# Kernel optimization log

Measured on AMD Instinct MI355X. Metric: run time of the kernel, lower is better.

The kernel has to match this reference:

```python
import jax, jax.numpy as jnp
import numpy as np

N = 50000
E = 800000
IN_C = 512
HID = 256
NUM_CLASS = (10, 25, 16, 350)


def _glorot(key, shape):
    fan_in, fan_out = shape[0], shape[1]
    lim = float(np.sqrt(6.0 / (fan_in + fan_out)))
    return jax.random.uniform(key, shape, jnp.float32, -lim, lim)


def setup_inputs() -> dict:
    key = jax.random.key(0)
    ks = jax.random.split(key, 16)
    x = jax.random.normal(ks[0], (N, IN_C), jnp.float32)
    edge_index = jax.random.randint(ks[1], (2, E), 0, N, jnp.int32)
    inp = {"x": x, "edge_index": edge_index}
    # gc1
    inp["W1"] = _glorot(ks[2], (IN_C, HID)); inp["b1"] = jnp.zeros((HID,), jnp.float32)
    # four GCNConv heads
    names = ["type", "school", "time", "author"]
    for i, (nm, nc) in enumerate(zip(names, NUM_CLASS)):
        inp[f"Wg_{nm}"] = _glorot(ks[3 + i], (HID, nc))
        inp[f"bg_{nm}"] = jnp.zeros((nc,), jnp.float32)
        inp[f"Wc_{nm}"] = _glorot(ks[7 + i], (nc, nc))
        inp[f"bc_{nm}"] = jnp.zeros((nc,), jnp.float32)
    return inp


def gcn_conv(x, W, b, src, dst, n):
    # GCNConv: out = D^{-1/2} (A + I) D^{-1/2} (x W) + b, symmetric norm.
    xw = x @ W  # [N, out]
    ones = jnp.ones((src.shape[0],), xw.dtype)
    deg = jax.ops.segment_sum(ones, dst, num_segments=n) + 1.0  # +1 from self-loop
    dinv = jax.lax.rsqrt(deg)
    norm = dinv[src] * dinv[dst]  # [E]
    agg = jax.ops.segment_sum(xw[src] * norm[:, None], dst, num_segments=n)
    # self-loop contribution: norm_ii = dinv_i^2
    return agg + xw * (dinv * dinv)[:, None] + b


def reference(x, edge_index, W1, b1,
              Wg_type, bg_type, Wc_type, bc_type,
              Wg_school, bg_school, Wc_school, bc_school,
              Wg_time, bg_time, Wc_time, bc_time,
              Wg_author, bg_author, Wc_author, bc_author):
    src, dst = edge_index[0], edge_index[1]
    n = x.shape[0]
    h = jax.nn.relu(gcn_conv(x, W1, b1, src, dst, n))  # dropout is identity in eval

    def head(Wg, bg, Wc, bc):
        g = gcn_conv(h, Wg, bg, src, dst, n)
        return jax.nn.softmax(g @ Wc + bc, axis=-1)

    out_type = head(Wg_type, bg_type, Wc_type, bc_type)
    out_school = head(Wg_school, bg_school, Wc_school, bc_school)
    out_time = head(Wg_time, bg_time, Wc_time, bc_time)
    out_author = head(Wg_author, bg_author, Wc_author, bc_author)
    return (out_type, out_school, out_time, out_author)
```

## Files before the change

### kernel.cpp

```cpp
#include <hip/hip_runtime.h>
#include <hip/hip_bf16.h>
#include <cstdint>
#include <cstddef>
#include <math.h>

#define NN 50000
#define NE 800000
#define INC 512
#define HIDC 256
#define NBLK ((NN + 255) / 256)
#define NB_DEG ((NE + 255) / 256)
#define NB_TR2 ((350 * 350 + 255) / 256)

typedef __attribute__((ext_vector_type(8))) short s8v;
typedef __attribute__((ext_vector_type(4))) float f4v;

__device__ __forceinline__ float b2f(unsigned short u) {
    return __uint_as_float(((unsigned)u) << 16);
}
__device__ __forceinline__ unsigned short f2b(float f) {
    __hip_bfloat16 h = __float2bfloat16(f);
    return *reinterpret_cast<unsigned short*>(&h);
}

__global__ void k_front1(const int* __restrict__ dst, int* __restrict__ cnt,
                         const float* __restrict__ Wg3, const float* __restrict__ Wc3,
                         float* __restrict__ Wg3t, float* __restrict__ Wc3t)
{
    if (blockIdx.x < NB_DEG) {
        int i = blockIdx.x * 256 + threadIdx.x;
        if (i < NE) atomicAdd(&cnt[dst[i]], 1);
    } else {
        int t = (blockIdx.x - NB_DEG) * 256 + threadIdx.x;
        if (t < 256 * 350) { int k = t / 350, i = t - k * 350; Wg3t[i * 256 + k] = Wg3[t]; }
        if (t < 350 * 350) { int i = t / 350, j = t - i * 350; Wc3t[j * 350 + i] = Wc3[t]; }
    }
}

__global__ void k_front2(const int* __restrict__ cnt, int* __restrict__ excl,
                         int* __restrict__ bsum, float* __restrict__ dinv,
                         const float* __restrict__ W1,
                         const float* __restrict__ Wg0, const float* __restrict__ Wc0,
                         const float* __restrict__ bg0, const float* __restrict__ bc0,
                         const float* __restrict__ Wg1, const float* __restrict__ Wc1,
                         const float* __restrict__ bg1, const float* __restrict__ bc1,
                         const float* __restrict__ Wg2, const float* __restrict__ Wc2,
                         const float* __restrict__ bg2, const float* __restrict__ bc2,
                         const float* __restrict__ Wg3, const float* __restrict__ Wc3,
                         const float* __restrict__ bg3, const float* __restrict__ bc3,
                         const float* __restrict__ Wg3t, const float* __restrict__ Wc3t,
                         unsigned short* __restrict__ W1t, unsigned short* __restrict__ Wft,
                         float* __restrict__ bfv)
{
    __shared__ float shm[352];
    int tid = threadIdx.x;
    if (blockIdx.x < NBLK) {
        int* s = (int*)shm;
        int i = blockIdx.x * 256 + tid;
        int v = (i < NN) ? cnt[i] : 0;
        if (i < NN) dinv[i] = rsqrtf((float)v + 1.0f);
        s[tid] = v;
        __syncthreads();
        for (int off = 1; off < 256; off <<= 1) {
            int t = (tid >= off) ? s[tid - off] : 0;
            __syncthreads();
            s[tid] += t;
            __syncthreads();
        }
        if (i < NN) excl[i] = s[tid] - v;
        if (tid == 255) bsum[blockIdx.x] = s[255];
        return;
    }
    int b = blockIdx.x - NBLK;
    if (b < 512) {
        int t = b * 256 + tid;
        int c = t >> 9, k = t & 511;
        W1t[(size_t)c * 512 + k] = f2b(W1[(size_t)k * 256 + c]);
    } else if (b < 960) {
        int j = b - 512, k = tid;
        float s = 0.f;
        if (j < 350) {
            for (int i = tid; i < 350; i += 256) shm[i] = Wc3t[(size_t)j * 350 + i];
            __syncthreads();
            for (int i = 0; i < 350; ++i) s += Wg3t[i * 256 + k] * shm[i];
        } else if (j >= 352 && j < 362) {
            int jj = j - 352; for (int i = 0; i < 10; ++i) s += Wg0[k * 10 + i] * Wc0[i * 10 + jj];
        } else if (j >= 362 && j < 387) {
            int jj = j - 362; for (int i = 0; i < 25; ++i) s += Wg1[k * 25 + i] * Wc1[i * 25 + jj];
        } else if (j >= 387 && j < 403) {
            int jj = j - 387; for (int i = 0; i < 16; ++i) s += Wg2[k * 16 + i] * Wc2[i * 16 + jj];
        }
        Wft[(size_t)j * 256 + k] = f2b(s);
    } else {
        int j = (b - 960) * 256 + tid;
        if (j >= 448) return;
        float s = 0.f;
        if (j < 350)                  { s = bc3[j]; for (int i = 0; i < 350; ++i) s += bg3[i] * Wc3[(size_t)i * 350 + j]; }
        else if (j >= 352 && j < 362) { int jj = j - 352; s = bc0[jj]; for (int i = 0; i < 10; ++i) s += bg0[i] * Wc0[i * 10 + jj]; }
        else if (j >= 362 && j < 387) { int jj = j - 362; s = bc1[jj]; for (int i = 0; i < 25; ++i) s += bg1[i] * Wc1[i * 25 + jj]; }
        else if (j >= 387 && j < 403) { int jj = j - 387; s = bc2[jj]; for (int i = 0; i < 16; ++i) s += bg2[i] * Wc2[i * 16 + jj]; }
        bfv[j] = s;
    }
}

#define GEMM1_NB ((NN + 127) / 128)
__global__ __launch_bounds__(512) void k_front3(
    const float* __restrict__ X, const unsigned short* __restrict__ Bt,
    unsigned short* __restrict__ C,
    int* __restrict__ rowptr, const int* __restrict__ bsum, int M)
{
    __shared__ s8v As[1024];
    __shared__ s8v Bs[2048];
    const int t = threadIdx.x;

    if (blockIdx.x >= GEMM1_NB) {
        int* sred = (int*)As;
        int b = blockIdx.x - GEMM1_NB;
        int v = (t < b) ? bsum[t] : 0;
        for (int o = 32; o; o >>= 1) v += __shfl_xor(v, o);
        if ((t & 63) == 0) sred[t >> 6] = v;
        __syncthreads();
        int off = 0;
#pragma unroll
        for (int w = 0; w < 8; ++w) off += sred[w];
        if (t < 256) {
            int i = b * 256 + t;
            if (i < NN) rowptr[i] += off;
            if (i == 0) rowptr[NN] = NE;
        }
        return;
    }

    const int lane = t & 63, wv = t >> 6;
    const int row0 = blockIdx.x * 128;
    const int l15 = lane & 15, lq = lane >> 4, l7 = lane & 7;

    f4v acc[16] = {};
    for (int k0 = 0; k0 < 512; k0 += 64) {
#pragma unroll
        for (int s = 0; s < 2; ++s) {
            int c = s * 512 + t;
            int row = c >> 3, ch = c & 7;
            int chg = ch ^ (row & 7);
            int gr = row0 + row; if (gr >= M) gr = M - 1;
            const float* src = X + (size_t)gr * 512 + k0 + chg * 8;
            float4 a = *(const float4*)src;
            float4 b = *(const float4*)(src + 4);
            s8v o;
            o[0] = (short)f2b(a.x); o[1] = (short)f2b(a.y);
            o[2] = (short)f2b(a.z); o[3] = (short)f2b(a.w);
            o[4] = (short)f2b(b.x); o[5] = (short)f2b(b.y);
            o[6] = (short)f2b(b.z); o[7] = (short)f2b(b.w);
            As[c] = o;
        }
#pragma unroll
        for (int s = 0; s < 4; ++s) {
            int c = s * 512 + t;
            int colr = c >> 3, ch = c & 7;
            int chg = ch ^ (colr & 7);
            Bs[c] = *(const s8v*)(Bt + (size_t)colr * 512 + k0 + chg * 8);
        }
        __syncthreads();
#pragma unroll
        for (int kk = 0; kk < 2; ++kk) {
            s8v af = As[(wv * 16 + l15) * 8 + ((kk * 4 + lq) ^ l7)];
#pragma unroll
            for (int cf = 0; cf < 16; ++cf) {
                s8v bfr = Bs[(cf * 16 + l15) * 8 + ((kk * 4 + lq) ^ l7)];
                acc[cf] = __builtin_amdgcn_mfma_f32_16x16x32_bf16(af, bfr, acc[cf], 0, 0, 0);
            }
        }
        __syncthreads();
    }
#pragma unroll
    for (int cf = 0; cf < 16; ++cf)
#pragma unroll
        for (int r = 0; r < 4; ++r) {
            int row = row0 + wv * 16 + lq * 4 + r;
            if (row < M) C[(size_t)row * 256 + cf * 16 + l15] = f2b(acc[cf][r]);
        }
}

__global__ void k_fill(const int* __restrict__ src, const int* __restrict__ dst,
                       const int* __restrict__ rowptr, int* __restrict__ cursor,
                       int* __restrict__ col, int e) {
    int i = blockIdx.x * 256 + threadIdx.x;
    if (i >= e) return;
    int d = dst[i];
    int pos = rowptr[d] + atomicAdd(&cursor[d], 1);
    col[pos] = src[i];
}

template <bool RELU, bool BIAS>
__global__ __launch_bounds__(256) void k_gather2(
    const unsigned short* __restrict__ feat, const int* __restrict__ rowptr,
    const int* __restrict__ col, const float* __restrict__ dinv,
    const float* __restrict__ bias, unsigned short* __restrict__ out, int n)
{
    int unit = (blockIdx.x * 256 + threadIdx.x) >> 5;
    int l32 = threadIdx.x & 31;
    if (unit >= n) return;
    float di = dinv[unit];
    int p0 = rowptr[unit], p1 = rowptr[unit + 1];
    int deg = p1 - p0;
    int myc = 0; float mydj = 0.f;
    if (l32 < deg) { myc = col[p0 + l32]; mydj = dinv[myc]; }
    float acc[8] = {};
    int dmin = deg < 32 ? deg : 32;
    int base = threadIdx.x & 32;
#pragma unroll 8
    for (int q = 0; q < dmin; ++q) {
        int j = __shfl(myc, base + q);
        float dj = __shfl(mydj, base + q);
        s8v v = *(const s8v*)(feat + (size_t)j * HIDC + l32 * 8);
#pragma unroll
        for (int c = 0; c < 8; ++c) acc[c] += dj * b2f((unsigned short)v[c]);
    }
    for (int p = p0 + 32; p < p1; ++p) {
        int j = col[p];
        float dj = dinv[j];
        s8v v = *(const s8v*)(feat + (size_t)j * HIDC + l32 * 8);
#pragma unroll
        for (int c = 0; c < 8; ++c) acc[c] += dj * b2f((unsigned short)v[c]);
    }
    s8v sv = *(const s8v*)(feat + (size_t)unit * HIDC + l32 * 8);
    float dd = di * di;
    s8v o;
#pragma unroll
    for (int c = 0; c < 8; ++c) {
        float r = di * acc[c] + dd * b2f((unsigned short)sv[c]);
        if (BIAS) r += bias[l32 * 8 + c];
        if (RELU) r = fmaxf(r, 0.f);
        o[c] = (short)f2b(r);
    }
    *(s8v*)(out + (size_t)unit * HIDC + l32 * 8) = o;
}

__global__ __launch_bounds__(512) void gemm2_heads(
    const unsigned short* __restrict__ A, const unsigned short* __restrict__ Bt,
    const float* __restrict__ bfv,
    float* __restrict__ o0, float* __restrict__ o1,
    float* __restrict__ o2, float* __restrict__ o3, int M)
{
    __shared__ s8v As[1024];
    __shared__ s8v Bs[3584];
    const int t = threadIdx.x;
    const int lane = t & 63, wv = t >> 6;
    const int row0 = blockIdx.x * 128;
    const int l15 = lane & 15, lq = lane >> 4, l7 = lane & 7;

    f4v acc[28] = {};
    for (int k0 = 0; k0 < 256; k0 += 64) {
#pragma unroll
        for (int s = 0; s < 2; ++s) {
            int c = s * 512 + t;
            int row = c >> 3, ch = c & 7;
            int chg = ch ^ (row & 7);
            int gr = row0 + row; if (gr >= M) gr = M - 1;
            As[c] = *(const s8v*)(A + (size_t)gr * 256 + k0 + chg * 8);
        }
#pragma unroll
        for (int s = 0; s < 7; ++s) {
            int c = s * 512 + t;
            int colr = c >> 3, ch = c & 7;
            int chg = ch ^ (colr & 7);
            Bs[c] = *(const s8v*)(Bt + (size_t)colr * 256 + k0 + chg * 8);
        }
        __syncthreads();
#pragma unroll
        for (int kk = 0; kk < 2; ++kk) {
            s8v af = As[(wv * 16 + l15) * 8 + ((kk * 4 + lq) ^ l7)];
#pragma unroll
            for (int cf = 0; cf < 28; ++cf) {
                s8v bfr = Bs[(cf * 16 + l15) * 8 + ((kk * 4 + lq) ^ l7)];
                acc[cf] = __builtin_amdgcn_mfma_f32_16x16x32_bf16(af, bfr, acc[cf], 0, 0, 0);
            }
        }
        __syncthreads();
    }
#pragma unroll
    for (int cf = 0; cf < 28; ++cf) {
        float b = bfv[cf * 16 + l15];
#pragma unroll
        for (int r = 0; r < 4; ++r) acc[cf][r] += b;
    }
#pragma unroll
    for (int r = 0; r < 4; ++r) {
        int row = row0 + wv * 16 + lq * 4 + r;
        float m0 = -1e30f, m1 = -1e30f, m2 = -1e30f, m3 = -1e30f;
#pragma unroll
        for (int cf = 0; cf < 28; ++cf) {
            int colc = cf * 16 + l15;
            float xv = acc[cf][r];
            if (colc < 350) m0 = fmaxf(m0, xv);
            else if (colc >= 352 && colc < 362) m1 = fmaxf(m1, xv);
            else if (colc >= 362 && colc < 387) m2 = fmaxf(m2, xv);
            else if (colc >= 387 && colc < 403) m3 = fmaxf(m3, xv);
        }
#pragma unroll
        for (int o = 8; o; o >>= 1) {
            m0 = fmaxf(m0, __shfl_xor(m0, o));
            m1 = fmaxf(m1, __shfl_xor(m1, o));
            m2 = fmaxf(m2, __shfl_xor(m2, o));
            m3 = fmaxf(m3, __shfl_xor(m3, o));
        }
        float s0 = 0.f, s1 = 0.f, s2 = 0.f, s3 = 0.f;
#pragma unroll
        for (int cf = 0; cf < 28; ++cf) {
            int colc = cf * 16 + l15;
            float xv = acc[cf][r];
            float e = 0.f;
            if (colc < 350)                     { e = __expf(xv - m0); s0 += e; }
            else if (colc >= 352 && colc < 362) { e = __expf(xv - m1); s1 += e; }
            else if (colc >= 362 && colc < 387) { e = __expf(xv - m2); s2 += e; }
            else if (colc >= 387 && colc < 403) { e = __expf(xv - m3); s3 += e; }
            acc[cf][r] = e;
        }
#pragma unroll
        for (int o = 8; o; o >>= 1) {
            s0 += __shfl_xor(s0, o); s1 += __shfl_xor(s1, o);
            s2 += __shfl_xor(s2, o); s3 += __shfl_xor(s3, o);
        }
        float i0 = 1.f / s0, i1 = 1.f / s1, i2 = 1.f / s2, i3 = 1.f / s3;
        if (row < M) {
#pragma unroll
            for (int cf = 0; cf < 28; ++cf) {
                int colc = cf * 16 + l15;
                float e = acc[cf][r];
                if (colc < 350)                     o3[(size_t)row * 350 + colc]       = e * i0;
                else if (colc >= 352 && colc < 362) o0[(size_t)row * 10 + colc - 352]  = e * i1;
                else if (colc >= 362 && colc < 387) o1[(size_t)row * 25 + colc - 362]  = e * i2;
                else if (colc >= 387 && colc < 403) o2[(size_t)row * 16 + colc - 387]  = e * i3;
            }
        }
    }
}

extern "C" void kernel_launch(void* const* d_in, const int* in_sizes, int n_in,
                              void* d_out, int out_size, void* d_ws, size_t ws_size,
                              hipStream_t stream)
{
    const float* x   = (const float*)d_in[0];
    const int*   ei  = (const int*)d_in[1];
    const float* W1  = (const float*)d_in[2];
    const float* b1  = (const float*)d_in[3];
    const float* Wg0 = (const float*)d_in[4];
    const float* bg0 = (const float*)d_in[5];
    const float* Wc0 = (const float*)d_in[6];
    const float* bc0 = (const float*)d_in[7];
    const float* Wg1 = (const float*)d_in[8];
    const float* bg1 = (const float*)d_in[9];
    const float* Wc1 = (const float*)d_in[10];
    const float* bc1 = (const float*)d_in[11];
    const float* Wg2 = (const float*)d_in[12];
    const float* bg2 = (const float*)d_in[13];
    const float* Wc2 = (const float*)d_in[14];
    const float* bc2 = (const float*)d_in[15];
    const float* Wg3 = (const float*)d_in[16];
    const float* bg3 = (const float*)d_in[17];
    const float* Wc3 = (const float*)d_in[18];
    const float* bc3 = (const float*)d_in[19];
    const int* srcI = ei;
    const int* dstI = ei + NE;

    char* ws = (char*)d_ws;
    size_t off = 0;
    auto alloc = [&](size_t bytes) { void* p = ws + off; off += (bytes + 255) & ~(size_t)255; return p; };
    float* dinv   = (float*)alloc(50176 * 4);
    int*   rowptr = (int*)  alloc(50432 * 4);
    int*   cnt    = (int*)  alloc(2 * 50176 * 4);
    int*   cursor = cnt + 50176;
    int*   bsum   = (int*)  alloc(1024);
    int*   col    = (int*)  alloc((size_t)NE * 4);
    unsigned short* W1t = (unsigned short*)alloc(256 * 512 * 2);
    unsigned short* Wft = (unsigned short*)alloc(448 * 256 * 2);
    float* bfv   = (float*)alloc(448 * 4);
    float* Wg3t  = (float*)alloc(350 * 256 * 4);
    float* Wc3t  = (float*)alloc(350 * 350 * 4);
    unsigned short* xwb = (unsigned short*)alloc((size_t)NN * HIDC * 2);
    unsigned short* hb  = (unsigned short*)alloc((size_t)NN * HIDC * 2);
    unsigned short* ahb = xwb;

    float* out0 = (float*)d_out;
    float* out1 = out0 + (size_t)NN * 10;
    float* out2 = out1 + (size_t)NN * 25;
    float* out3 = out2 + (size_t)NN * 16;

    hipMemsetAsync(cnt, 0, 2 * 50176 * 4, stream);

    k_front1<<<NB_DEG + NB_TR2, 256, 0, stream>>>(dstI, cnt, Wg3, Wc3, Wg3t, Wc3t);
    k_front2<<<NBLK + 962, 256, 0, stream>>>(cnt, rowptr, bsum, dinv, W1,
                                             Wg0, Wc0, bg0, bc0, Wg1, Wc1, bg1, bc1,
                                             Wg2, Wc2, bg2, bc2, Wg3, Wc3, bg3, bc3,
                                             Wg3t, Wc3t, W1t, Wft, bfv);
    k_front3<<<GEMM1_NB + NBLK, 512, 0, stream>>>(x, W1t, xwb, rowptr, bsum, NN);
    k_fill<<<NB_DEG, 256, 0, stream>>>(srcI, dstI, rowptr, cursor, col, NE);

    k_gather2<true, true><<<(NN + 7) / 8, 256, 0, stream>>>(xwb, rowptr, col, dinv, b1, hb, NN);
    k_gather2<false, false><<<(NN + 7) / 8, 256, 0, stream>>>(hb, rowptr, col, dinv, nullptr, ahb, NN);
    gemm2_heads<<<(NN + 127) / 128, 512, 0, stream>>>(ahb, Wft, bfv, out0, out1, out2, out3, NN);
}
```

Before: 311.2 us.

## Split scan into own kernel and fuse CSR fill into GEMM1 launch

Moves the rowptr block-offset scan out of the GEMM1 kernel into a small separate kernel. The CSR column-fill step, which previously ran as its own kernel after GEMM1, now runs in extra blocks of the GEMM1 launch. The aim is to overlap the atomic-heavy edge scatter with the dense X·W1 GEMM instead of serializing them. The number of launches stays the same, but the scan now becomes a separate tiny serialized kernel, and the fill blocks compete with GEMM blocks for CUs.

```diff
diff --git a/kernel.cpp b/kernel.cpp
--- a/kernel.cpp
+++ b/kernel.cpp
@@ -103,30 +103,38 @@
     }
 }
 
+__global__ void k_scan3(int* __restrict__ rowptr, const int* __restrict__ bsum, int n, int e) {
+    __shared__ int sred[4];
+    int b = blockIdx.x, t = threadIdx.x;
+    int v = (t < b) ? bsum[t] : 0;
+    for (int o = 32; o; o >>= 1) v += __shfl_xor(v, o);
+    if ((t & 63) == 0) sred[t >> 6] = v;
+    __syncthreads();
+    int off = sred[0] + sred[1] + sred[2] + sred[3];
+    int i = b * 256 + t;
+    if (i < n) rowptr[i] += off;
+    if (i == 0) rowptr[n] = e;
+}
+
 #define GEMM1_NB ((NN + 127) / 128)
-__global__ __launch_bounds__(512) void k_front3(
+#define FILL_NB ((NE + 511) / 512)
+__global__ __launch_bounds__(512) void k_front4(
     const float* __restrict__ X, const unsigned short* __restrict__ Bt,
     unsigned short* __restrict__ C,
-    int* __restrict__ rowptr, const int* __restrict__ bsum, int M)
+    const int* __restrict__ src, const int* __restrict__ dst,
+    const int* __restrict__ rowptr, int* __restrict__ cursor,
+    int* __restrict__ col, int M)
 {
     __shared__ s8v As[1024];
     __shared__ s8v Bs[2048];
     const int t = threadIdx.x;
 
     if (blockIdx.x >= GEMM1_NB) {
-        int* sred = (int*)As;
-        int b = blockIdx.x - GEMM1_NB;
-        int v = (t < b) ? bsum[t] : 0;
-        for (int o = 32; o; o >>= 1) v += __shfl_xor(v, o);
-        if ((t & 63) == 0) sred[t >> 6] = v;
-        __syncthreads();
-        int off = 0;
-#pragma unroll
-        for (int w = 0; w < 8; ++w) off += sred[w];
-        if (t < 256) {
-            int i = b * 256 + t;
-            if (i < NN) rowptr[i] += off;
-            if (i == 0) rowptr[NN] = NE;
+        int i = (blockIdx.x - GEMM1_NB) * 512 + t;
+        if (i < NE) {
+            int d = dst[i];
+            int pos = rowptr[d] + atomicAdd(&cursor[d], 1);
+            col[pos] = src[i];
         }
         return;
     }
@@ -143,9 +151,9 @@
             int row = c >> 3, ch = c & 7;
             int chg = ch ^ (row & 7);
             int gr = row0 + row; if (gr >= M) gr = M - 1;
-            const float* src = X + (size_t)gr * 512 + k0 + chg * 8;
-            float4 a = *(const float4*)src;
-            float4 b = *(const float4*)(src + 4);
+            const float* srcp = X + (size_t)gr * 512 + k0 + chg * 8;
+            float4 a = *(const float4*)srcp;
+            float4 b = *(const float4*)(srcp + 4);
             s8v o;
             o[0] = (short)f2b(a.x); o[1] = (short)f2b(a.y);
             o[2] = (short)f2b(a.z); o[3] = (short)f2b(a.w);
@@ -179,16 +187,6 @@
             int row = row0 + wv * 16 + lq * 4 + r;
             if (row < M) C[(size_t)row * 256 + cf * 16 + l15] = f2b(acc[cf][r]);
         }
-}
-
-__global__ void k_fill(const int* __restrict__ src, const int* __restrict__ dst,
-                       const int* __restrict__ rowptr, int* __restrict__ cursor,
-                       int* __restrict__ col, int e) {
-    int i = blockIdx.x * 256 + threadIdx.x;
-    if (i >= e) return;
-    int d = dst[i];
-    int pos = rowptr[d] + atomicAdd(&cursor[d], 1);
-    col[pos] = src[i];
 }
 
 template <bool RELU, bool BIAS>
@@ -393,8 +391,9 @@
                                              Wg0, Wc0, bg0, bc0, Wg1, Wc1, bg1, bc1,
                                              Wg2, Wc2, bg2, bc2, Wg3, Wc3, bg3, bc3,
                                              Wg3t, Wc3t, W1t, Wft, bfv);
-    k_front3<<<GEMM1_NB + NBLK, 512, 0, stream>>>(x, W1t, xwb, rowptr, bsum, NN);
-    k_fill<<<NB_DEG, 256, 0, stream>>>(srcI, dstI, rowptr, cursor, col, NE);
+    k_scan3<<<NBLK, 256, 0, stream>>>(rowptr, bsum, NN, NE);
+    k_front4<<<GEMM1_NB + FILL_NB, 512, 0, stream>>>(x, W1t, xwb, srcI, dstI,
+                                                     rowptr, cursor, col, NN);
 
     k_gather2<true, true><<<(NN + 7) / 8, 256, 0, stream>>>(xwb, rowptr, col, dinv, b1, hb, NN);
     k_gather2<false, false><<<(NN + 7) / 8, 256, 0, stream>>>(hb, rowptr, col, dinv, nullptr, ahb, NN);
```

Measured after the change: 302.6 us. 1.03x faster.
